# Performance work log

Hardware: AMD Instinct MI355X
Metric: run time of the kernel (lower is better)

Reference implementation:

```python
import jax, jax.numpy as jnp
import numpy as np
from jax import lax

_SQ2 = np.sqrt(2.0)
_H2 = (np.array([[1.0, 1.0], [1.0, -1.0]]) / _SQ2).astype(np.complex64)
_BN_INV = 1.0 / np.sqrt(1.0 + 1e-5)  # eval-mode BN, running_mean=0, running_var=1

# wire 0 is the most-significant bit of the 4-qubit basis index (PennyLane convention)
def _cnot_perm(c, t):
    p = np.arange(16)
    for b in range(16):
        if (b >> (3 - c)) & 1:
            p[b] = b ^ (1 << (3 - t))
    return p

# CNOT(0,1) then CNOT(1,2) then CNOT(2,3) then CNOT(3,0); psi_out = psi_in[perm]
_p01, _p12, _p23, _p30 = _cnot_perm(0, 1), _cnot_perm(1, 2), _cnot_perm(2, 3), _cnot_perm(3, 0)
_PTOT = _p01[_p12[_p23[_p30]]]
# PauliZ expectation signs: (16 basis states, 4 wires)
_ZM = np.array([[1.0 - 2.0 * ((b >> (3 - w)) & 1) for w in range(4)] for b in range(16)], np.float32)


def _make_unitaries(w0, w1):
    """w0, w1: (C,2). Circuit: H^4 -> RY(w0[0],w0[1],w0[0],w0[1]) -> RZ(w1 same pattern) -> CNOT ring."""
    ty = jnp.stack([w0[:, 0], w0[:, 1], w0[:, 0], w0[:, 1]], axis=1)  # (C,4)
    tz = jnp.stack([w1[:, 0], w1[:, 1], w1[:, 0], w1[:, 1]], axis=1)
    c, s = jnp.cos(ty / 2), jnp.sin(ty / 2)
    ry = jnp.stack([jnp.stack([c, -s], -1), jnp.stack([s, c], -1)], -2).astype(jnp.complex64)  # (C,4,2,2)
    ph = jnp.exp(-0.5j * tz.astype(jnp.complex64))  # (C,4)
    zr = jnp.zeros_like(ph)
    rz = jnp.stack([jnp.stack([ph, zr], -1), jnp.stack([zr, jnp.conj(ph)], -1)], -2)  # (C,4,2,2)
    g = rz @ ry @ jnp.asarray(_H2)  # per-wire single-qubit gate, (C,4,2,2)
    U = g[:, 0]
    for w in range(1, 4):  # kron over wires 0..3
        d = U.shape[1]
        U = jnp.einsum('cij,ckl->cikjl', U, g[:, w]).reshape(U.shape[0], d * 2, d * 2)
    return U[:, _PTOT, :]  # fold the CNOT-ring permutation into U


def _conv_bn_relu(x, w, g, b):
    y = lax.conv_general_dilated(x, w, (1, 1), ((1, 1), (1, 1)),
                                 dimension_numbers=('NCHW', 'OIHW', 'NCHW'))
    y = y * (g * _BN_INV)[None, :, None, None] + b[None, :, None, None]
    return jax.nn.relu(y)


def _bn_relu(x, g, b):
    return jax.nn.relu(x * (g * _BN_INV)[None, :, None, None] + b[None, :, None, None])


def _maxpool2(x):
    return lax.reduce_window(x, -jnp.inf, lax.max, (1, 1, 2, 2), (1, 1, 2, 2), 'VALID')


def _quantum_stage(e4, q_w0, q_w1):
    B, C, H, W = e4.shape
    xp = jnp.pad(e4, ((0, 0), (0, 0), (1, 2), (1, 2)))  # F.pad(1,2,1,2)
    # 4x4 patches, stride 1, row-major (matches torch unfold->view ordering): (B,C,H,W,16)
    patches = jnp.stack([xp[:, :, i:i + H, j:j + W] for i in range(4) for j in range(4)], axis=-1)
    nrm = jnp.sqrt(jnp.sum(patches * patches, axis=-1, keepdims=True))
    psi0 = (patches / jnp.maximum(nrm, 1e-12)).astype(jnp.complex64)  # AmplitudeEmbedding(normalize=True)
    U = _make_unitaries(q_w0, q_w1)  # (C,16,16) complex
    psi = jnp.einsum('cij,bchwj->bchwi', U, psi0)
    probs = psi.real ** 2 + psi.imag ** 2
    ev = jnp.einsum('bchwi,iq->bchwq', probs, jnp.asarray(_ZM))  # <Z_w> per wire
    return (ev.mean(-1) + 1.0) / 2.0


def setup_inputs() -> dict:
    key = jax.random.key(0)
    ks = jax.random.split(key, 18)
    conv_w = lambda k, o, i: jax.random.normal(k, (o, i, 3, 3), jnp.float32) / np.sqrt(i * 9)
    gamma = lambda k, c: jax.random.uniform(k, (c,), jnp.float32, 0.75, 1.25)
    beta = lambda k, c: 0.1 * jax.random.normal(k, (c,), jnp.float32)
    return {
        'x': jax.random.normal(ks[0], (8, 1, 256, 256), jnp.float32),
        'w1': conv_w(ks[1], 32, 1), 'g1': gamma(ks[2], 32), 'b1': beta(ks[3], 32),
        'w2': conv_w(ks[4], 64, 32), 'g2': gamma(ks[5], 64), 'b2': beta(ks[6], 64),
        'w3': conv_w(ks[7], 128, 64), 'g3': gamma(ks[8], 128), 'b3': beta(ks[9], 128),
        'w4': conv_w(ks[10], 256, 128), 'g4': gamma(ks[11], 256), 'b4': beta(ks[12], 256),
        'q_w0': 0.5 * jax.random.normal(ks[13], (256, 2), jnp.float32),
        'q_w1': 0.5 * jax.random.normal(ks[14], (256, 2), jnp.float32),
        'g5': gamma(ks[15], 256), 'b5': beta(ks[16], 256),
    }


def reference(x, w1, g1, b1, w2, g2, b2, w3, g3, b3, w4, g4, b4, q_w0, q_w1, g5, b5):
    e1 = _conv_bn_relu(x, w1, g1, b1)                 # (8,32,256,256)
    e2 = _conv_bn_relu(_maxpool2(e1), w2, g2, b2)     # (8,64,128,128)
    e3 = _conv_bn_relu(_maxpool2(e2), w3, g3, b3)     # (8,128,64,64)
    e4 = _conv_bn_relu(_maxpool2(e3), w4, g4, b4)     # (8,256,32,32)
    q = _quantum_stage(e4, q_w0, q_w1)                # (8,256,32,32)
    out4 = _bn_relu(q, g5, b5)
    return (e1, e2, e3, out4)
```

## Files before the change

### kernel.cpp

```cpp
#include <hip/hip_runtime.h>
#include <cstdint>
#include <cstddef>

#define BN_INV 0.9999950000374997f

typedef __attribute__((ext_vector_type(8))) _Float16 h8v;
typedef __attribute__((ext_vector_type(4))) float f4v;

__device__ __forceinline__ void fsplit(float v, ushort& h, ushort& l) {
    _Float16 hh = (_Float16)v;
    _Float16 ll = (_Float16)(v - (float)hh);
    h = __builtin_bit_cast(ushort, hh);
    l = __builtin_bit_cast(ushort, ll);
}

__device__ __forceinline__ void repack_one(
    const float* __restrict__ w, ushort* __restrict__ dst, int CIN, int i)
{
    int ocf = i / (CIN * 9);
    int r = i % (CIN * 9);
    int ic = r / 9;
    int tap = r % 9;
    int ocg = ocf >> 6, oc = ocf & 63;
    int chunk = ic >> 5, q = (ic >> 3) & 3, j = ic & 7;
    int nch = CIN >> 5;
    ushort h, l;
    fsplit(w[i], h, l);
    size_t base = (size_t)((ocg * nch + chunk) * 2) * 18432
                + (size_t)tap * 2048 + q * 512 + oc * 8 + j;
    dst[base] = h;
    dst[base + 18432] = l;
}

__global__ __launch_bounds__(256) void prep_conv1_kernel(
    const float* __restrict__ w0, const float* __restrict__ w1,
    float* __restrict__ U,
    const float* __restrict__ w2, ushort* __restrict__ wb2,
    const float* __restrict__ w3, ushort* __restrict__ wb3,
    const float* __restrict__ w4, ushort* __restrict__ wb4,
    const float* __restrict__ x, const float* __restrict__ wt,
    const float* __restrict__ g, const float* __restrict__ be,
    float* __restrict__ out, ushort* __restrict__ pooled)
{
    __shared__ float s_in[18][18];
    __shared__ float s_w[288];

    int blk = blockIdx.x;
    int tid = threadIdx.x;

    if (blk < 1528) {
        if (blk >= 376)      { repack_one(w4, wb4, 128, (blk - 376) * 256 + tid); return; }
        if (blk >= 88)       { repack_one(w3, wb3,  64, (blk -  88) * 256 + tid); return; }
        if (blk >= 16)       { repack_one(w2, wb2,  32, (blk -  16) * 256 + tid); return; }

        int idx = blk * 256 + tid;
        int c = idx >> 4, r = idx & 15;
        float gr[4][2][2], gi[4][2][2];
        const float inv_sq2 = 0.70710678118654752f;
#pragma unroll
        for (int w = 0; w < 4; ++w) {
            float ty = w0[c * 2 + (w & 1)];
            float tz = w1[c * 2 + (w & 1)];
            float cy = cosf(0.5f * ty), sy = sinf(0.5f * ty);
            float cz = cosf(0.5f * tz), sz = sinf(0.5f * tz);
            float r00 = (cy - sy) * inv_sq2, r01 = (cy + sy) * inv_sq2;
            float r10 = (cy + sy) * inv_sq2, r11 = (sy - cy) * inv_sq2;
            gr[w][0][0] = cz * r00; gi[w][0][0] = -sz * r00;
            gr[w][0][1] = cz * r01; gi[w][0][1] = -sz * r01;
            gr[w][1][0] = cz * r10; gi[w][1][0] =  sz * r10;
            gr[w][1][1] = cz * r11; gi[w][1][1] =  sz * r11;
        }
        const int PTOT[16] = {0,13,3,14,6,11,5,8,12,1,15,2,10,7,9,4};
        int rp = PTOT[r];
        float* Uo = U + (size_t)c * 512 + r * 32;
#pragma unroll
        for (int cc = 0; cc < 16; ++cc) {
            float pr = 1.f, pi = 0.f;
#pragma unroll
            for (int w = 0; w < 4; ++w) {
                int ib = (rp >> (3 - w)) & 1, jb = (cc >> (3 - w)) & 1;
                float ar = gr[w][ib][jb], ai = gi[w][ib][jb];
                float nr = pr * ar - pi * ai;
                float ni = pr * ai + pi * ar;
                pr = nr; pi = ni;
            }
            Uo[cc * 2 + 0] = pr;
            Uo[cc * 2 + 1] = pi;
        }
        return;
    }

    int bid = blk - 1528;
    int tile = bid & 255;
    int b = bid >> 8;
    int tx0 = (tile & 15) * 16, ty0 = (tile >> 4) * 16;

    for (int i = tid; i < 288; i += 256) s_w[i] = wt[i];
    for (int i = tid; i < 18 * 18; i += 256) {
        int yy = i / 18, xx = i % 18;
        int gy = ty0 + yy - 1, gx = tx0 + xx - 1;
        float v = 0.f;
        if (gy >= 0 && gy < 256 && gx >= 0 && gx < 256)
            v = x[(size_t)b * 65536 + gy * 256 + gx];
        s_in[yy][xx] = v;
    }
    __syncthreads();

    int px = tid & 15, py = tid >> 4;
    float t[3][3];
#pragma unroll
    for (int i = 0; i < 3; ++i)
#pragma unroll
        for (int j = 0; j < 3; ++j) t[i][j] = s_in[py + i][px + j];

    bool wr_pool = ((px & 1) == 0) && ((py & 1) == 0);
    ushort ph[32], pl[32];

    size_t obase = ((size_t)b * 32) * 65536 + (size_t)(ty0 + py) * 256 + (tx0 + px);
#pragma unroll 4
    for (int oc = 0; oc < 32; ++oc) {
        const float* wr = &s_w[oc * 9];
        float s = wr[0]*t[0][0] + wr[1]*t[0][1] + wr[2]*t[0][2]
                + wr[3]*t[1][0] + wr[4]*t[1][1] + wr[5]*t[1][2]
                + wr[6]*t[2][0] + wr[7]*t[2][1] + wr[8]*t[2][2];
        s = s * (g[oc] * BN_INV) + be[oc];
        s = fmaxf(s, 0.f);
        out[obase + (size_t)oc * 65536] = s;
        float p = fmaxf(s, __shfl_xor(s, 1));
        p = fmaxf(p, __shfl_xor(p, 16));
        fsplit(p, ph[oc], pl[oc]);
    }
    if (wr_pool) {
        ushort* op = pooled + (((size_t)b * 128 + ((ty0 + py) >> 1)) * 128 + ((tx0 + px) >> 1)) * 64;
#pragma unroll
        for (int k = 0; k < 4; ++k) {
            uint4 u;
            u.x = (uint)ph[8*k+0] | ((uint)ph[8*k+1] << 16);
            u.y = (uint)ph[8*k+2] | ((uint)ph[8*k+3] << 16);
            u.z = (uint)ph[8*k+4] | ((uint)ph[8*k+5] << 16);
            u.w = (uint)ph[8*k+6] | ((uint)ph[8*k+7] << 16);
            *(uint4*)(op + 8 * k) = u;
            uint4 v;
            v.x = (uint)pl[8*k+0] | ((uint)pl[8*k+1] << 16);
            v.y = (uint)pl[8*k+2] | ((uint)pl[8*k+3] << 16);
            v.z = (uint)pl[8*k+4] | ((uint)pl[8*k+5] << 16);
            v.w = (uint)pl[8*k+6] | ((uint)pl[8*k+7] << 16);
            *(uint4*)(op + 32 + 8 * k) = v;
        }
    }
}

template <int CIN, int COUT, int HW, bool POOL>
__global__ __launch_bounds__(256) void conv3x3_mfma_split(
    const ushort* __restrict__ in,
    const ushort* __restrict__ wb,
    const float* __restrict__ g, const float* __restrict__ be,
    float* __restrict__ out,
    ushort* __restrict__ pooled)
{
    constexpr int NCH = CIN / 32;
    constexpr int NTX = HW / 16;
    constexpr int NT = NTX * (HW / 8);
    constexpr int NOCG = COUT / 64;
    constexpr int PS = 72;

    __shared__ __align__(16) ushort s_in[180 * PS];

    int bid = blockIdx.x;
    int tile = bid % NT;
    int rest = bid / NT;
    int ocg = rest % NOCG;
    int b = rest / NOCG;
    int x0 = (tile % NTX) * 16;
    int y0 = (tile / NTX) * 8;

    int tid = threadIdx.x;
    int wv = tid >> 6;
    int lane = tid & 63;
    int n = lane & 15;
    int q = lane >> 4;
    int oc_half = (wv & 1) * 32;
    int sg = wv >> 1;

    int ib[4];
#pragma unroll
    for (int f = 0; f < 4; ++f)
        ib[f] = ((sg * 4 + f) * 18 + n) * PS + q * 8;
    int iwa0 = q * 512 + (oc_half + n) * 8;
    int iwa1 = q * 512 + (oc_half + 16 + n) * 8;

    const ushort* inb = in + (size_t)b * HW * HW * 2 * CIN;

    f4v acc[2][4];
#pragma unroll
    for (int a = 0; a < 2; ++a)
#pragma unroll
        for (int f = 0; f < 4; ++f) acc[a][f] = (f4v){0.f, 0.f, 0.f, 0.f};

    for (int ch = 0; ch < NCH; ++ch) {
        if (ch) __syncthreads();
#pragma unroll
        for (int it = 0; it < 12; ++it) {
            int i = tid + it * 256;
            if (i < 2880) {
                int pos = i >> 4;
                int r2 = i & 15;
                int comp = r2 >> 3;
                int u = r2 & 7;
                int py = pos / 18, px = pos % 18;
                int gy = y0 - 1 + py, gx = x0 - 1 + px;
                uint2 v; v.x = 0u; v.y = 0u;
                if (gy >= 0 && gy < HW && gx >= 0 && gx < HW)
                    v = *(const uint2*)(inb + ((size_t)gy * HW + gx) * (2 * CIN)
                                        + comp * CIN + ch * 32 + u * 4);
                *(uint2*)(&s_in[pos * PS + comp * 32 + u * 4]) = v;
            }
        }
        __syncthreads();

        const ushort* wc = wb + (size_t)((ocg * NCH + ch) * 2) * 18432;
#pragma unroll 3
        for (int tap = 0; tap < 9; ++tap) {
            const int toff = ((tap / 3) * 18 + (tap % 3)) * PS;
            const ushort* wt_ = wc + tap * 2048;
            h8v ah0 = *(const h8v*)(wt_ + iwa0);
            h8v ah1 = *(const h8v*)(wt_ + iwa1);
            h8v al0 = *(const h8v*)(wt_ + 18432 + iwa0);
            h8v al1 = *(const h8v*)(wt_ + 18432 + iwa1);
            h8v bh[4], bl[4];
#pragma unroll
            for (int f = 0; f < 4; ++f) {
                bh[f] = *(const h8v*)(&s_in[toff + ib[f]]);
                bl[f] = *(const h8v*)(&s_in[toff + ib[f] + 32]);
            }
#pragma unroll
            for (int f = 0; f < 4; ++f) {
                acc[0][f] = __builtin_amdgcn_mfma_f32_16x16x32_f16(ah0, bh[f], acc[0][f], 0, 0, 0);
                acc[1][f] = __builtin_amdgcn_mfma_f32_16x16x32_f16(ah1, bh[f], acc[1][f], 0, 0, 0);
            }
#pragma unroll
            for (int f = 0; f < 4; ++f) {
                acc[0][f] = __builtin_amdgcn_mfma_f32_16x16x32_f16(ah0, bl[f], acc[0][f], 0, 0, 0);
                acc[1][f] = __builtin_amdgcn_mfma_f32_16x16x32_f16(ah1, bl[f], acc[1][f], 0, 0, 0);
            }
#pragma unroll
            for (int f = 0; f < 4; ++f) {
                acc[0][f] = __builtin_amdgcn_mfma_f32_16x16x32_f16(al0, bh[f], acc[0][f], 0, 0, 0);
                acc[1][f] = __builtin_amdgcn_mfma_f32_16x16x32_f16(al1, bh[f], acc[1][f], 0, 0, 0);
            }
        }
    }

    float vr[2][4][4];
#pragma unroll
    for (int tf = 0; tf < 2; ++tf)
#pragma unroll
        for (int f = 0; f < 4; ++f) {
            int y = y0 + sg * 4 + f;
#pragma unroll
            for (int r = 0; r < 4; ++r) {
                int oc = ocg * 64 + oc_half + tf * 16 + q * 4 + r;
                float v = fmaxf(acc[tf][f][r] * (g[oc] * BN_INV) + be[oc], 0.f);
                vr[tf][f][r] = v;
                out[((size_t)(b * COUT + oc) * HW + y) * HW + (x0 + n)] = v;
            }
        }

    if (POOL) {
#pragma unroll
        for (int tf = 0; tf < 2; ++tf)
#pragma unroll
            for (int fp = 0; fp < 2; ++fp) {
                ushort h[4], l[4];
#pragma unroll
                for (int r = 0; r < 4; ++r) {
                    float p = fmaxf(vr[tf][2 * fp][r], vr[tf][2 * fp + 1][r]);
                    p = fmaxf(p, __shfl_xor(p, 1));
                    fsplit(p, h[r], l[r]);
                }
                if ((n & 1) == 0) {
                    int pyp = (y0 >> 1) + sg * 2 + fp;
                    int pxp = (x0 + n) >> 1;
                    int ocb = ocg * 64 + oc_half + tf * 16 + q * 4;
                    ushort* op = pooled
                        + (((size_t)b * (HW / 2) + pyp) * (HW / 2) + pxp) * (2 * COUT);
                    uint2 uh, ul;
                    uh.x = (uint)h[0] | ((uint)h[1] << 16);
                    uh.y = (uint)h[2] | ((uint)h[3] << 16);
                    ul.x = (uint)l[0] | ((uint)l[1] << 16);
                    ul.y = (uint)l[2] | ((uint)l[3] << 16);
                    *(uint2*)(op + ocb) = uh;
                    *(uint2*)(op + COUT + ocb) = ul;
                }
            }
    }
}

__global__ __launch_bounds__(256) void quantum_bn_relu(
    const float* __restrict__ e4,
    const float* __restrict__ U,
    const float* __restrict__ g5, const float* __restrict__ b5,
    float* __restrict__ out)
{
    int blk = blockIdx.x;
    int c = blk & 255;
    __shared__ float sp[32][32];
    __shared__ __align__(16) float sU[512];

    int tid = threadIdx.x;
    const float4* plane4 = (const float4*)(e4 + (size_t)blk * 1024);
    ((float4*)sp)[tid] = plane4[tid];
    const float4* Usrc = (const float4*)(U + (size_t)c * 512);
    if (tid < 128) ((float4*)sU)[tid] = Usrc[tid];
    __syncthreads();

    float t[4][16];
    float inv2[4];
#pragma unroll
    for (int k = 0; k < 4; ++k) {
        int site = tid + 256 * k;
        int y = site >> 5, x = site & 31;
        float ss = 0.f;
#pragma unroll
        for (int i = 0; i < 4; ++i)
#pragma unroll
            for (int j = 0; j < 4; ++j) {
                int yy = y + i - 1, xx = x + j - 1;
                float v = (yy >= 0 && yy < 32 && xx >= 0 && xx < 32) ? sp[yy][xx] : 0.f;
                t[k][i * 4 + j] = v;
                ss += v * v;
            }
        float inv = 1.f / fmaxf(sqrtf(ss), 1e-12f);
        inv2[k] = inv * inv;
    }

    const int   RI[10] = {0, 1, 2, 4, 7, 8, 11, 13, 14, 15};
    const float ZM[10] = {1.f, .5f, .5f, .5f, -.5f, .5f, -.5f, -.5f, -.5f, -1.f};
    const float4* sU4 = (const float4*)sU;

    float s[4] = {0.f, 0.f, 0.f, 0.f};
#pragma unroll
    for (int ii = 0; ii < 10; ++ii) {
        int i = RI[ii];
        float re[4] = {0.f, 0.f, 0.f, 0.f};
        float im[4] = {0.f, 0.f, 0.f, 0.f};
#pragma unroll
        for (int jj = 0; jj < 8; ++jj) {
            float4 u = sU4[i * 8 + jj];
#pragma unroll
            for (int k = 0; k < 4; ++k) {
                re[k] += u.x * t[k][2 * jj];
                im[k] += u.y * t[k][2 * jj];
                re[k] += u.z * t[k][2 * jj + 1];
                im[k] += u.w * t[k][2 * jj + 1];
            }
        }
        float zm = ZM[ii];
#pragma unroll
        for (int k = 0; k < 4; ++k)
            s[k] += (re[k] * re[k] + im[k] * im[k]) * zm;
    }

    float sc = g5[c] * BN_INV, bi = b5[c];
#pragma unroll
    for (int k = 0; k < 4; ++k) {
        float q = (s[k] * inv2[k] + 1.f) * 0.5f;
        float o = fmaxf(q * sc + bi, 0.f);
        out[(size_t)blk * 1024 + tid + 256 * k] = o;
    }
}

extern "C" void kernel_launch(void* const* d_in, const int* in_sizes, int n_in,
                              void* d_out, int out_size, void* d_ws, size_t ws_size,
                              hipStream_t stream)
{
    const float* x   = (const float*)d_in[0];
    const float* w1  = (const float*)d_in[1];
    const float* g1  = (const float*)d_in[2];
    const float* b1  = (const float*)d_in[3];
    const float* w2  = (const float*)d_in[4];
    const float* g2  = (const float*)d_in[5];
    const float* b2  = (const float*)d_in[6];
    const float* w3  = (const float*)d_in[7];
    const float* g3  = (const float*)d_in[8];
    const float* b3  = (const float*)d_in[9];
    const float* w4  = (const float*)d_in[10];
    const float* g4  = (const float*)d_in[11];
    const float* b4  = (const float*)d_in[12];
    const float* qw0 = (const float*)d_in[13];
    const float* qw1 = (const float*)d_in[14];
    const float* g5  = (const float*)d_in[15];
    const float* b5  = (const float*)d_in[16];

    float* out = (float*)d_out;
    float* e1  = out;
    float* e2  = out + 16777216;
    float* e3  = out + 25165824;
    float* o4  = out + 29360128;

    float* ws = (float*)d_ws;
    float*  Uw  = ws;
    ushort* wb2 = (ushort*)(ws + 131072);
    ushort* wb3 = (ushort*)(ws + 149504);
    ushort* wb4 = (ushort*)(ws + 223232);
    ushort* pt1 = (ushort*)(ws + 518144);
    ushort* pt2 = (ushort*)(ws + 4712448);
    ushort* pt3 = (ushort*)(ws + 518144);

    prep_conv1_kernel<<<1528 + 2048, 256, 0, stream>>>(
        qw0, qw1, Uw, w2, wb2, w3, wb3, w4, wb4,
        x, w1, g1, b1, e1, pt1);

    conv3x3_mfma_split<32, 64, 128, true><<<1024, 256, 0, stream>>>(pt1, wb2, g2, b2, e2, pt2);

    conv3x3_mfma_split<64, 128, 64, true><<<512, 256, 0, stream>>>(pt2, wb3, g3, b3, e3, pt3);

    conv3x3_mfma_split<128, 256, 32, false><<<256, 256, 0, stream>>>(pt3, wb4, g4, b4, o4, nullptr);

    quantum_bn_relu<<<2048, 256, 0, stream>>>(o4, Uw, g5, b5, o4);
}
```

Baseline: 296.8 us.

## Double-buffer conv input staging, use 512-thread blocks, reshape conv1 tiles, pad quantum plane

The MFMA conv kernels move to 512 threads, with each wave handling two rows instead of four. Input channel chunks are now double-buffered in shared memory so the next chunk loads while the current one computes. The change also adds an XCD-aware block-index remap and wave priority hints. Separately, conv1 switches to 32x8 tiles with the pool shuffle adjusted, and the quantum kernel zero-pads its plane in shared memory to remove bounds checks. The aim is better latency hiding and occupancy, at the cost of more LDS per block and a remap that assumes the grid size is divisible by 8.

```diff
diff --git a/kernel.cpp b/kernel.cpp
--- a/kernel.cpp
+++ b/kernel.cpp
@@ -42,7 +42,7 @@
     const float* __restrict__ g, const float* __restrict__ be,
     float* __restrict__ out, ushort* __restrict__ pooled)
 {
-    __shared__ float s_in[18][18];
+    __shared__ float s_in[10][34];
     __shared__ float s_w[288];
 
     int blk = blockIdx.x;
@@ -93,11 +93,11 @@
     int bid = blk - 1528;
     int tile = bid & 255;
     int b = bid >> 8;
-    int tx0 = (tile & 15) * 16, ty0 = (tile >> 4) * 16;
+    int tx0 = (tile & 7) * 32, ty0 = (tile >> 3) * 8;
 
     for (int i = tid; i < 288; i += 256) s_w[i] = wt[i];
-    for (int i = tid; i < 18 * 18; i += 256) {
-        int yy = i / 18, xx = i % 18;
+    for (int i = tid; i < 340; i += 256) {
+        int yy = i / 34, xx = i % 34;
         int gy = ty0 + yy - 1, gx = tx0 + xx - 1;
         float v = 0.f;
         if (gy >= 0 && gy < 256 && gx >= 0 && gx < 256)
@@ -106,7 +106,7 @@
     }
     __syncthreads();
 
-    int px = tid & 15, py = tid >> 4;
+    int px = tid & 31, py = tid >> 5;
     float t[3][3];
 #pragma unroll
     for (int i = 0; i < 3; ++i)
@@ -127,7 +127,7 @@
         s = fmaxf(s, 0.f);
         out[obase + (size_t)oc * 65536] = s;
         float p = fmaxf(s, __shfl_xor(s, 1));
-        p = fmaxf(p, __shfl_xor(p, 16));
+        p = fmaxf(p, __shfl_xor(p, 32));
         fsplit(p, ph[oc], pl[oc]);
     }
     if (wr_pool) {
@@ -151,7 +151,7 @@
 }
 
 template <int CIN, int COUT, int HW, bool POOL>
-__global__ __launch_bounds__(256) void conv3x3_mfma_split(
+__global__ __launch_bounds__(512) void conv3x3_mfma_split(
     const ushort* __restrict__ in,
     const ushort* __restrict__ wb,
     const float* __restrict__ g, const float* __restrict__ be,
@@ -163,10 +163,15 @@
     constexpr int NT = NTX * (HW / 8);
     constexpr int NOCG = COUT / 64;
     constexpr int PS = 72;
-
-    __shared__ __align__(16) ushort s_in[180 * PS];
-
+    constexpr int BUFSZ = 180 * PS;
+    constexpr int NBUF = (NCH > 1) ? 2 : 1;
+
+    __shared__ __align__(16) ushort s_in[NBUF * BUFSZ];
+
+    constexpr int NWG = NT * NOCG * 8;
     int bid = blockIdx.x;
+    bid = (bid & 7) * (NWG >> 3) + (bid >> 3);
+
     int tile = bid % NT;
     int rest = bid / NT;
     int ocg = rest % NOCG;
@@ -182,26 +187,25 @@
     int oc_half = (wv & 1) * 32;
     int sg = wv >> 1;
 
-    int ib[4];
-#pragma unroll
-    for (int f = 0; f < 4; ++f)
-        ib[f] = ((sg * 4 + f) * 18 + n) * PS + q * 8;
+    int ib[2];
+#pragma unroll
+    for (int f = 0; f < 2; ++f)
+        ib[f] = ((sg * 2 + f) * 18 + n) * PS + q * 8;
     int iwa0 = q * 512 + (oc_half + n) * 8;
     int iwa1 = q * 512 + (oc_half + 16 + n) * 8;
 
     const ushort* inb = in + (size_t)b * HW * HW * 2 * CIN;
 
-    f4v acc[2][4];
+    f4v acc[2][2];
 #pragma unroll
     for (int a = 0; a < 2; ++a)
 #pragma unroll
-        for (int f = 0; f < 4; ++f) acc[a][f] = (f4v){0.f, 0.f, 0.f, 0.f};
-
-    for (int ch = 0; ch < NCH; ++ch) {
-        if (ch) __syncthreads();
-#pragma unroll
-        for (int it = 0; it < 12; ++it) {
-            int i = tid + it * 256;
+        for (int f = 0; f < 2; ++f) acc[a][f] = (f4v){0.f, 0.f, 0.f, 0.f};
+
+    auto stage = [&](int ch, int bsel) {
+#pragma unroll
+        for (int it = 0; it < 6; ++it) {
+            int i = tid + it * 512;
             if (i < 2880) {
                 int pos = i >> 4;
                 int r2 = i & 15;
@@ -213,12 +217,20 @@
                 if (gy >= 0 && gy < HW && gx >= 0 && gx < HW)
                     v = *(const uint2*)(inb + ((size_t)gy * HW + gx) * (2 * CIN)
                                         + comp * CIN + ch * 32 + u * 4);
-                *(uint2*)(&s_in[pos * PS + comp * 32 + u * 4]) = v;
-            }
-        }
+                *(uint2*)(&s_in[bsel * BUFSZ + pos * PS + comp * 32 + u * 4]) = v;
+            }
+        }
+    };
+
+    stage(0, 0);
+    int cur = 0;
+    for (int ch = 0; ch < NCH; ++ch) {
         __syncthreads();
+        if (ch + 1 < NCH) stage(ch + 1, cur ^ 1);
 
         const ushort* wc = wb + (size_t)((ocg * NCH + ch) * 2) * 18432;
+        const ushort* sb = &s_in[cur * BUFSZ];
+        __builtin_amdgcn_s_setprio(1);
 #pragma unroll 3
         for (int tap = 0; tap < 9; ++tap) {
             const int toff = ((tap / 3) * 18 + (tap % 3)) * PS;
@@ -227,36 +239,38 @@
             h8v ah1 = *(const h8v*)(wt_ + iwa1);
             h8v al0 = *(const h8v*)(wt_ + 18432 + iwa0);
             h8v al1 = *(const h8v*)(wt_ + 18432 + iwa1);
-            h8v bh[4], bl[4];
-#pragma unroll
-            for (int f = 0; f < 4; ++f) {
-                bh[f] = *(const h8v*)(&s_in[toff + ib[f]]);
-                bl[f] = *(const h8v*)(&s_in[toff + ib[f] + 32]);
-            }
-#pragma unroll
-            for (int f = 0; f < 4; ++f) {
+            h8v bh[2], bl[2];
+#pragma unroll
+            for (int f = 0; f < 2; ++f) {
+                bh[f] = *(const h8v*)(&sb[toff + ib[f]]);
+                bl[f] = *(const h8v*)(&sb[toff + ib[f] + 32]);
+            }
+#pragma unroll
+            for (int f = 0; f < 2; ++f) {
                 acc[0][f] = __builtin_amdgcn_mfma_f32_16x16x32_f16(ah0, bh[f], acc[0][f], 0, 0, 0);
                 acc[1][f] = __builtin_amdgcn_mfma_f32_16x16x32_f16(ah1, bh[f], acc[1][f], 0, 0, 0);
             }
 #pragma unroll
-            for (int f = 0; f < 4; ++f) {
+            for (int f = 0; f < 2; ++f) {
                 acc[0][f] = __builtin_amdgcn_mfma_f32_16x16x32_f16(ah0, bl[f], acc[0][f], 0, 0, 0);
                 acc[1][f] = __builtin_amdgcn_mfma_f32_16x16x32_f16(ah1, bl[f], acc[1][f], 0, 0, 0);
             }
 #pragma unroll
-            for (int f = 0; f < 4; ++f) {
+            for (int f = 0; f < 2; ++f) {
                 acc[0][f] = __builtin_amdgcn_mfma_f32_16x16x32_f16(al0, bh[f], acc[0][f], 0, 0, 0);
                 acc[1][f] = __builtin_amdgcn_mfma_f32_16x16x32_f16(al1, bh[f], acc[1][f], 0, 0, 0);
             }
         }
-    }
-
-    float vr[2][4][4];
+        __builtin_amdgcn_s_setprio(0);
+        cur ^= (NBUF - 1);
+    }
+
+    float vr[2][2][4];
 #pragma unroll
     for (int tf = 0; tf < 2; ++tf)
 #pragma unroll
-        for (int f = 0; f < 4; ++f) {
-            int y = y0 + sg * 4 + f;
+        for (int f = 0; f < 2; ++f) {
+            int y = y0 + sg * 2 + f;
 #pragma unroll
             for (int r = 0; r < 4; ++r) {
                 int oc = ocg * 64 + oc_half + tf * 16 + q * 4 + r;
@@ -268,31 +282,29 @@
 
     if (POOL) {
 #pragma unroll
-        for (int tf = 0; tf < 2; ++tf)
-#pragma unroll
-            for (int fp = 0; fp < 2; ++fp) {
-                ushort h[4], l[4];
-#pragma unroll
-                for (int r = 0; r < 4; ++r) {
-                    float p = fmaxf(vr[tf][2 * fp][r], vr[tf][2 * fp + 1][r]);
-                    p = fmaxf(p, __shfl_xor(p, 1));
-                    fsplit(p, h[r], l[r]);
-                }
-                if ((n & 1) == 0) {
-                    int pyp = (y0 >> 1) + sg * 2 + fp;
-                    int pxp = (x0 + n) >> 1;
-                    int ocb = ocg * 64 + oc_half + tf * 16 + q * 4;
-                    ushort* op = pooled
-                        + (((size_t)b * (HW / 2) + pyp) * (HW / 2) + pxp) * (2 * COUT);
-                    uint2 uh, ul;
-                    uh.x = (uint)h[0] | ((uint)h[1] << 16);
-                    uh.y = (uint)h[2] | ((uint)h[3] << 16);
-                    ul.x = (uint)l[0] | ((uint)l[1] << 16);
-                    ul.y = (uint)l[2] | ((uint)l[3] << 16);
-                    *(uint2*)(op + ocb) = uh;
-                    *(uint2*)(op + COUT + ocb) = ul;
-                }
-            }
+        for (int tf = 0; tf < 2; ++tf) {
+            ushort h[4], l[4];
+#pragma unroll
+            for (int r = 0; r < 4; ++r) {
+                float p = fmaxf(vr[tf][0][r], vr[tf][1][r]);
+                p = fmaxf(p, __shfl_xor(p, 1));
+                fsplit(p, h[r], l[r]);
+            }
+            if ((n & 1) == 0) {
+                int pyp = (y0 >> 1) + sg;
+                int pxp = (x0 + n) >> 1;
+                int ocb = ocg * 64 + oc_half + tf * 16 + q * 4;
+                ushort* op = pooled
+                    + (((size_t)b * (HW / 2) + pyp) * (HW / 2) + pxp) * (2 * COUT);
+                uint2 uh, ul;
+                uh.x = (uint)h[0] | ((uint)h[1] << 16);
+                uh.y = (uint)h[2] | ((uint)h[3] << 16);
+                ul.x = (uint)l[0] | ((uint)l[1] << 16);
+                ul.y = (uint)l[2] | ((uint)l[3] << 16);
+                *(uint2*)(op + ocb) = uh;
+                *(uint2*)(op + COUT + ocb) = ul;
+            }
+        }
     }
 }
 
@@ -304,14 +316,22 @@
 {
     int blk = blockIdx.x;
     int c = blk & 255;
-    __shared__ float sp[32][32];
+    __shared__ float sp[35][35];
     __shared__ __align__(16) float sU[512];
 
     int tid = threadIdx.x;
-    const float4* plane4 = (const float4*)(e4 + (size_t)blk * 1024);
-    ((float4*)sp)[tid] = plane4[tid];
+    for (int i = tid; i < 1225; i += 256) ((float*)sp)[i] = 0.f;
     const float4* Usrc = (const float4*)(U + (size_t)c * 512);
     if (tid < 128) ((float4*)sU)[tid] = Usrc[tid];
+    float4 pv = ((const float4*)(e4 + (size_t)blk * 1024))[tid];
+    __syncthreads();
+    {
+        int y = tid >> 3, x4 = (tid & 7) << 2;
+        sp[y + 1][x4 + 1] = pv.x;
+        sp[y + 1][x4 + 2] = pv.y;
+        sp[y + 1][x4 + 3] = pv.z;
+        sp[y + 1][x4 + 4] = pv.w;
+    }
     __syncthreads();
 
     float t[4][16];
@@ -325,8 +345,7 @@
         for (int i = 0; i < 4; ++i)
 #pragma unroll
             for (int j = 0; j < 4; ++j) {
-                int yy = y + i - 1, xx = x + j - 1;
-                float v = (yy >= 0 && yy < 32 && xx >= 0 && xx < 32) ? sp[yy][xx] : 0.f;
+                float v = sp[y + i][x + j];
                 t[k][i * 4 + j] = v;
                 ss += v * v;
             }
@@ -411,11 +430,11 @@
         qw0, qw1, Uw, w2, wb2, w3, wb3, w4, wb4,
         x, w1, g1, b1, e1, pt1);
 
-    conv3x3_mfma_split<32, 64, 128, true><<<1024, 256, 0, stream>>>(pt1, wb2, g2, b2, e2, pt2);
-
-    conv3x3_mfma_split<64, 128, 64, true><<<512, 256, 0, stream>>>(pt2, wb3, g3, b3, e3, pt3);
-
-    conv3x3_mfma_split<128, 256, 32, false><<<256, 256, 0, stream>>>(pt3, wb4, g4, b4, o4, nullptr);
+    conv3x3_mfma_split<32, 64, 128, true><<<1024, 512, 0, stream>>>(pt1, wb2, g2, b2, e2, pt2);
+
+    conv3x3_mfma_split<64, 128, 64, true><<<512, 512, 0, stream>>>(pt2, wb3, g3, b3, e3, pt3);
+
+    conv3x3_mfma_split<128, 256, 32, false><<<256, 512, 0, stream>>>(pt3, wb4, g4, b4, o4, nullptr);
 
     quantum_bn_relu<<<2048, 256, 0, stream>>>(o4, Uw, g5, b5, o4);
 }
```

Result: faster. 281.2 us (-5.3%).
